# Kernel tuning notes

Hardware: AMD Instinct MI355X
Metric: run time of the kernel (lower is better)

## Reference

```python
import jax, jax.numpy as jnp
import numpy as np

EPS = 1e-5  # config.layer_norm_epsilon

def setup_inputs() -> dict:
    key = jax.random.key(0)
    ks = jax.random.split(key, 3)
    B, S, NX, A, H, O = 16, 2048, 1024, 20, 50, 3
    x = jax.random.normal(ks[0], (B, S, NX), dtype=jnp.float32)
    ln_g = jnp.ones((A, NX), jnp.float32)
    ln_b = jnp.zeros((A, NX), jnp.float32)
    W1 = jax.random.normal(ks[1], (A, NX, H), dtype=jnp.float32) * (1.0 / np.sqrt(NX))
    b1 = jnp.zeros((A, H), jnp.float32)
    W2 = jax.random.normal(ks[2], (A, H, O), dtype=jnp.float32) * (1.0 / np.sqrt(H))
    b2 = jnp.zeros((A, O), jnp.float32)
    return {"x": x, "ln_g": ln_g, "ln_b": ln_b, "W1": W1, "b1": b1, "W2": W2, "b2": b2}

def reference(x, ln_g, ln_b, W1, b1, W2, b2):
    B, S, NX = x.shape
    A = ln_g.shape[0]
    # shared normalization (per-token mean/var), per-adapter affine folded into W1
    mu = jnp.mean(x, axis=-1, keepdims=True)
    var = jnp.mean(jnp.square(x - mu), axis=-1, keepdims=True)  # biased, like torch LN
    xn = (x - mu) * jax.lax.rsqrt(var + EPS)                    # [B,S,NX]
    W1g = ln_g[:, :, None] * W1                                 # [A,NX,H], absorbs LN gamma
    off = jnp.einsum('an,anh->ah', ln_b, W1) + b1               # [A,H],   absorbs LN beta
    h = jax.nn.relu(jnp.einsum('bsn,anh->bash', xn, W1g) + off[None, :, None, :])  # [B,A,S,H]
    o = jnp.einsum('bash,aho->baso', h, W2) + b2[None, :, None, :]                 # [B,A,S,3]
    out = o.reshape(B, A, S * o.shape[-1])                      # [B,A,S*3] (row-major == torch view)
    # squash over the adapter/capsule axis (dim=-1 of [B,S*3,A] == axis 1 here)
    sq = jnp.sum(jnp.square(out), axis=1, keepdims=True)
    scale = sq / (1.0 + sq)
    return scale * out * jax.lax.rsqrt(sq)
```

## Files before the change

### kernel.cpp

```cpp
#include <hip/hip_runtime.h>
#include <hip/hip_bf16.h>
#include <stdint.h>


typedef _Float16 h8 __attribute__((ext_vector_type(8)));
typedef float f4 __attribute__((ext_vector_type(4)));
typedef __attribute__((address_space(1))) void gvoid;
typedef __attribute__((address_space(3))) void lvoid;

__device__ __forceinline__ void cp16(const void* g, void* l) {
  __builtin_amdgcn_global_load_lds((gvoid*)g, (lvoid*)l, 16, 0, 0);
}

__global__ __launch_bounds__(256) void ln_kernel(const float* __restrict__ x,
                                                 _Float16* __restrict__ xn) {
  const int t = threadIdx.x, w = t >> 6, l = t & 63;
  const int tok = blockIdx.x * 4 + w;
  const float4* xr = (const float4*)(x + (size_t)tok * 1024);
  float4 v0 = xr[l * 2], v1 = xr[l * 2 + 1];
  float4 v2 = xr[128 + l * 2], v3 = xr[128 + l * 2 + 1];
  float s1 = (v0.x + v0.y + v0.z + v0.w) + (v1.x + v1.y + v1.z + v1.w) +
             (v2.x + v2.y + v2.z + v2.w) + (v3.x + v3.y + v3.z + v3.w);
  float s2 = v0.x * v0.x + v0.y * v0.y + v0.z * v0.z + v0.w * v0.w;
  s2 += v1.x * v1.x + v1.y * v1.y + v1.z * v1.z + v1.w * v1.w;
  s2 += v2.x * v2.x + v2.y * v2.y + v2.z * v2.z + v2.w * v2.w;
  s2 += v3.x * v3.x + v3.y * v3.y + v3.z * v3.z + v3.w * v3.w;
#pragma unroll
  for (int m = 32; m > 0; m >>= 1) {
    s1 += __shfl_xor(s1, m);
    s2 += __shfl_xor(s2, m);
  }
  const float mu = s1 * 0.0009765625f;
  const float var = s2 * 0.0009765625f - mu * mu;
  const float inv = rsqrtf(var + 1e-5f);
  union { _Float16 h[8]; uint4 u; } p;
  _Float16* xw = xn + (size_t)tok * 1024 + l * 8;
  p.h[0] = (_Float16)((v0.x - mu) * inv); p.h[1] = (_Float16)((v0.y - mu) * inv);
  p.h[2] = (_Float16)((v0.z - mu) * inv); p.h[3] = (_Float16)((v0.w - mu) * inv);
  p.h[4] = (_Float16)((v1.x - mu) * inv); p.h[5] = (_Float16)((v1.y - mu) * inv);
  p.h[6] = (_Float16)((v1.z - mu) * inv); p.h[7] = (_Float16)((v1.w - mu) * inv);
  *(uint4*)xw = p.u;
  p.h[0] = (_Float16)((v2.x - mu) * inv); p.h[1] = (_Float16)((v2.y - mu) * inv);
  p.h[2] = (_Float16)((v2.z - mu) * inv); p.h[3] = (_Float16)((v2.w - mu) * inv);
  p.h[4] = (_Float16)((v3.x - mu) * inv); p.h[5] = (_Float16)((v3.y - mu) * inv);
  p.h[6] = (_Float16)((v3.z - mu) * inv); p.h[7] = (_Float16)((v3.w - mu) * inv);
  *(uint4*)(xw + 512) = p.u;
}

__global__ __launch_bounds__(256) void prep_w(const float* __restrict__ ln_g,
                                              const float* __restrict__ ln_b,
                                              const float* __restrict__ W1,
                                              _Float16* __restrict__ wB,
                                              float* __restrict__ offacc) {
  const int a = blockIdx.x, k0 = blockIdx.y * 64, t = threadIdx.x;
  __shared__ float tw[3200];
  __shared__ float gg[64], bb[64];
  const float* src = W1 + (size_t)(a * 1024 + k0) * 50;
  for (int i = t; i < 3200; i += 256) tw[i] = src[i];
  if (t < 64) gg[t] = ln_g[a * 1024 + k0 + t];
  else if (t < 128) bb[t - 64] = ln_b[a * 1024 + k0 + (t - 64)];
  __syncthreads();
  const int h = t & 63, q = t >> 6;
  float po = 0.f;
#pragma unroll
  for (int half = 0; half < 2; ++half) {
    union { _Float16 hh[8]; uint4 u; } pk;
#pragma unroll
    for (int j = 0; j < 8; ++j) {
      const int k = q * 16 + half * 8 + j;
      float wv = (h < 50) ? tw[k * 50 + h] : 0.f;
      pk.hh[j] = (_Float16)(gg[k] * wv);
      po += bb[k] * wv;
    }
    *(uint4*)(wB + (size_t)(a * 64 + h) * 1024 + k0 + q * 16 + half * 8) =
        pk.u;
  }
  if (h < 50 && po != 0.f) atomicAdd(&offacc[a * 64 + h], po);
}

__global__ __launch_bounds__(256, 4) void gemm_kernel(
    const _Float16* __restrict__ xn, const _Float16* __restrict__ wB,
    const float* __restrict__ offacc, const float* __restrict__ b1,
    const float* __restrict__ W2, const float* __restrict__ b2,
    float* __restrict__ out) {
  __shared__ __align__(16) char smem[35280];
  const int nb = blockIdx.x, mb = blockIdx.y;
  const int t = threadIdx.x, w = t >> 6, l = t & 63;

  float* w2s = (float*)(smem + 34048);
  for (int i = t; i < 300; i += 256) w2s[i] = W2[nb * 300 + i];
  if (t < 6) w2s[300 + t] = b2[nb * 6 + t];

  const int lr = l >> 3;
  const int ksl = (l & 7) ^ lr;
  const _Float16* gA = xn + (size_t)(mb * 128 + lr) * 1024 + ksl * 8;
  const _Float16* gB = wB + (size_t)(nb * 128 + lr) * 1024 + ksl * 8;

  const int rowA = ((w >> 1) * 64) + (l & 15);
  const int rowB = ((w & 1) * 64) + (l & 15);
  const int kq = l >> 4;
  const int xa = rowA & 7, xb = rowB & 7;
  const char* pA = smem + rowA * 128;
  const char* pB = smem + 16384 + rowB * 128;

  f4 acc[4][4];
  {
    f4 z = {0.f, 0.f, 0.f, 0.f};
#pragma unroll
    for (int mt = 0; mt < 4; ++mt)
#pragma unroll
      for (int nt = 0; nt < 4; ++nt) acc[mt][nt] = z;
  }

  for (int kt = 0; kt < 16; ++kt) {
#pragma unroll
    for (int i = 0; i < 4; ++i) {
      const int chunk = w * 4 + i;
      cp16(gA + (size_t)chunk * 8192 + kt * 64, smem + chunk * 1024);
      cp16(gB + (size_t)chunk * 8192 + kt * 64, smem + 16384 + chunk * 1024);
    }
    __syncthreads();
#pragma unroll
    for (int ks = 0; ks < 2; ++ks) {
      h8 af[4], bf[4];
      const int sl = ks * 4 + kq;
#pragma unroll
      for (int mt = 0; mt < 4; ++mt)
        af[mt] = *(const h8*)(pA + mt * 2048 + ((sl ^ xa) << 4));
#pragma unroll
      for (int nt = 0; nt < 4; ++nt)
        bf[nt] = *(const h8*)(pB + nt * 2048 + ((sl ^ xb) << 4));
#pragma unroll
      for (int mt = 0; mt < 4; ++mt)
#pragma unroll
        for (int nt = 0; nt < 4; ++nt)
          acc[mt][nt] = __builtin_amdgcn_mfma_f32_16x16x32_f16(
              af[mt], bf[nt], acc[mt][nt], 0, 0, 0);
    }
    __syncthreads();
  }

  float offt[4];
#pragma unroll
  for (int nt = 0; nt < 4; ++nt) {
    const int nc = rowB + nt * 16;
    const int hh = nc & 63;
    float bv = (hh < 50) ? b1[(nb * 2 + (nc >> 6)) * 50 + hh] : 0.f;
    offt[nt] = offacc[nb * 128 + nc] + bv;
  }

  float* hm = (float*)smem;
  const int mrl = (l >> 4) * 4;
  const int ncol = (w & 1) * 64 + (l & 15);
#pragma unroll
  for (int p = 0; p < 2; ++p) {
    if (p) __syncthreads();
    if ((w >> 1) == p) {
#pragma unroll
      for (int mt = 0; mt < 4; ++mt)
#pragma unroll
        for (int nt = 0; nt < 4; ++nt)
#pragma unroll
          for (int r = 0; r < 4; ++r)
            hm[(mrl + mt * 16 + r) * 133 + (ncol + nt * 16)] =
                fmaxf(acc[mt][nt][r] + offt[nt], 0.f);
    }
    __syncthreads();
    if (t < 128) {
      const int ml = t >> 1, pr = t & 1;
      const float* hrow = hm + ml * 133 + pr * 64;
      const float* wrow = w2s + pr * 150;
      float o0 = w2s[300 + pr * 3 + 0];
      float o1 = w2s[300 + pr * 3 + 1];
      float o2 = w2s[300 + pr * 3 + 2];
#pragma unroll 10
      for (int h = 0; h < 50; ++h) {
        const float hv = hrow[h];
        o0 += hv * wrow[h * 3 + 0];
        o1 += hv * wrow[h * 3 + 1];
        o2 += hv * wrow[h * 3 + 2];
      }
      const int tok = mb * 128 + p * 64 + ml;
      const int b = tok >> 11, s = tok & 2047;
      const int ag = nb * 2 + pr;
      float* op = out + ((size_t)(b * 20 + ag) * 2048 + (size_t)s) * 3;
      op[0] = o0; op[1] = o1; op[2] = o2;
    }
  }
}

__global__ __launch_bounds__(256) void squash_kernel(float* __restrict__ out) {
  const int idx = blockIdx.x * 256 + threadIdx.x;
  const int b = idx / 6144;
  const int rem = idx - b * 6144;
  float v[20];
  float sq = 0.f;
#pragma unroll
  for (int a = 0; a < 20; ++a) {
    v[a] = out[((size_t)(b * 20 + a)) * 6144 + rem];
    sq += v[a] * v[a];
  }
  const float f = sqrtf(sq) / (1.f + sq);
#pragma unroll
  for (int a = 0; a < 20; ++a)
    out[((size_t)(b * 20 + a)) * 6144 + rem] = v[a] * f;
}

extern "C" void kernel_launch(void* const* d_in, const int* in_sizes, int n_in,
                              void* d_out, int out_size, void* d_ws,
                              size_t ws_size, hipStream_t stream) {
  const float* x    = (const float*)d_in[0];
  const float* ln_g = (const float*)d_in[1];
  const float* ln_b = (const float*)d_in[2];
  const float* W1   = (const float*)d_in[3];
  const float* b1   = (const float*)d_in[4];
  const float* W2   = (const float*)d_in[5];
  const float* b2   = (const float*)d_in[6];
  float* out = (float*)d_out;

  char* ws = (char*)d_ws;
  float* offacc = (float*)ws;
  _Float16* wB  = (_Float16*)(ws + 8192);
  _Float16* xnw = (_Float16*)(ws + 8192 + 2621440);

  hipMemsetAsync(offacc, 0, 1280 * sizeof(float), stream);
  prep_w<<<dim3(20, 16), 256, 0, stream>>>(ln_g, ln_b, W1, wB, offacc);
  ln_kernel<<<8192, 256, 0, stream>>>(x, xnw);
  gemm_kernel<<<dim3(10, 256), 256, 0, stream>>>(xnw, wB, offacc, b1, W2, b2, out);
  squash_kernel<<<384, 256, 0, stream>>>(out);
}
```

Measured before the change: 317.6 us.

## Pack adapter columns densely and fuse LayerNorm normalization into GEMM A-tile loads

```diff
diff --git a/kernel.cpp b/kernel.cpp
--- a/kernel.cpp
+++ b/kernel.cpp
@@ -12,39 +12,29 @@
   __builtin_amdgcn_global_load_lds((gvoid*)g, (lvoid*)l, 16, 0, 0);
 }
 
-__global__ __launch_bounds__(256) void ln_kernel(const float* __restrict__ x,
-                                                 _Float16* __restrict__ xn) {
+__global__ __launch_bounds__(256) void stats_kernel(const float* __restrict__ x,
+                                                    float2* __restrict__ st) {
   const int t = threadIdx.x, w = t >> 6, l = t & 63;
   const int tok = blockIdx.x * 4 + w;
   const float4* xr = (const float4*)(x + (size_t)tok * 1024);
-  float4 v0 = xr[l * 2], v1 = xr[l * 2 + 1];
-  float4 v2 = xr[128 + l * 2], v3 = xr[128 + l * 2 + 1];
-  float s1 = (v0.x + v0.y + v0.z + v0.w) + (v1.x + v1.y + v1.z + v1.w) +
-             (v2.x + v2.y + v2.z + v2.w) + (v3.x + v3.y + v3.z + v3.w);
-  float s2 = v0.x * v0.x + v0.y * v0.y + v0.z * v0.z + v0.w * v0.w;
-  s2 += v1.x * v1.x + v1.y * v1.y + v1.z * v1.z + v1.w * v1.w;
-  s2 += v2.x * v2.x + v2.y * v2.y + v2.z * v2.z + v2.w * v2.w;
-  s2 += v3.x * v3.x + v3.y * v3.y + v3.z * v3.z + v3.w * v3.w;
+  float s1 = 0.f, s2 = 0.f;
+#pragma unroll
+  for (int i = 0; i < 4; ++i) {
+    float4 v = xr[l + i * 64];
+    s1 += v.x + v.y + v.z + v.w;
+    s2 += v.x * v.x + v.y * v.y + v.z * v.z + v.w * v.w;
+  }
 #pragma unroll
   for (int m = 32; m > 0; m >>= 1) {
     s1 += __shfl_xor(s1, m);
     s2 += __shfl_xor(s2, m);
   }
-  const float mu = s1 * 0.0009765625f;
-  const float var = s2 * 0.0009765625f - mu * mu;
-  const float inv = rsqrtf(var + 1e-5f);
-  union { _Float16 h[8]; uint4 u; } p;
-  _Float16* xw = xn + (size_t)tok * 1024 + l * 8;
-  p.h[0] = (_Float16)((v0.x - mu) * inv); p.h[1] = (_Float16)((v0.y - mu) * inv);
-  p.h[2] = (_Float16)((v0.z - mu) * inv); p.h[3] = (_Float16)((v0.w - mu) * inv);
-  p.h[4] = (_Float16)((v1.x - mu) * inv); p.h[5] = (_Float16)((v1.y - mu) * inv);
-  p.h[6] = (_Float16)((v1.z - mu) * inv); p.h[7] = (_Float16)((v1.w - mu) * inv);
-  *(uint4*)xw = p.u;
-  p.h[0] = (_Float16)((v2.x - mu) * inv); p.h[1] = (_Float16)((v2.y - mu) * inv);
-  p.h[2] = (_Float16)((v2.z - mu) * inv); p.h[3] = (_Float16)((v2.w - mu) * inv);
-  p.h[4] = (_Float16)((v3.x - mu) * inv); p.h[5] = (_Float16)((v3.y - mu) * inv);
-  p.h[6] = (_Float16)((v3.z - mu) * inv); p.h[7] = (_Float16)((v3.w - mu) * inv);
-  *(uint4*)(xw + 512) = p.u;
+  if (l == 0) {
+    const float mu = s1 * 0.0009765625f;
+    const float var = s2 * 0.0009765625f - mu * mu;
+    const float inv = rsqrtf(var + 1e-5f);
+    st[tok] = make_float2(inv, -mu * inv);
+  }
 }
 
 __global__ __launch_bounds__(256) void prep_w(const float* __restrict__ ln_g,
@@ -61,39 +51,53 @@
   else if (t < 128) bb[t - 64] = ln_b[a * 1024 + k0 + (t - 64)];
   __syncthreads();
   const int h = t & 63, q = t >> 6;
-  float po = 0.f;
-#pragma unroll
-  for (int half = 0; half < 2; ++half) {
-    union { _Float16 hh[8]; uint4 u; } pk;
-#pragma unroll
-    for (int j = 0; j < 8; ++j) {
-      const int k = q * 16 + half * 8 + j;
-      float wv = (h < 50) ? tw[k * 50 + h] : 0.f;
-      pk.hh[j] = (_Float16)(gg[k] * wv);
-      po += bb[k] * wv;
-    }
-    *(uint4*)(wB + (size_t)(a * 64 + h) * 1024 + k0 + q * 16 + half * 8) =
-        pk.u;
-  }
-  if (h < 50 && po != 0.f) atomicAdd(&offacc[a * 64 + h], po);
+  if (h < 50) {
+    float po = 0.f;
+#pragma unroll
+    for (int half = 0; half < 2; ++half) {
+      union { _Float16 hh[8]; uint4 u; } pk;
+#pragma unroll
+      for (int j = 0; j < 8; ++j) {
+        const int k = q * 16 + half * 8 + j;
+        const float wv = tw[k * 50 + h];
+        pk.hh[j] = (_Float16)(gg[k] * wv);
+        po += bb[k] * wv;
+      }
+      *(uint4*)(wB + (size_t)(a * 50 + h) * 1024 + k0 + q * 16 + half * 8) =
+          pk.u;
+    }
+    if (po != 0.f) atomicAdd(&offacc[a * 50 + h], po);
+  }
+  if (a == 0 && t < 192) {
+    const uint4 z = {0, 0, 0, 0};
+    *(uint4*)(wB + (size_t)(1000 + (t >> 3)) * 1024 + k0 + (t & 7) * 8) = z;
+  }
 }
 
 __global__ __launch_bounds__(256, 4) void gemm_kernel(
-    const _Float16* __restrict__ xn, const _Float16* __restrict__ wB,
-    const float* __restrict__ offacc, const float* __restrict__ b1,
-    const float* __restrict__ W2, const float* __restrict__ b2,
+    const float* __restrict__ x, const float2* __restrict__ st,
+    const _Float16* __restrict__ wB, const float* __restrict__ offacc,
+    const float* __restrict__ b1, const float* __restrict__ W2,
     float* __restrict__ out) {
-  __shared__ __align__(16) char smem[35280];
+  __shared__ __align__(16) char smem[36448];
   const int nb = blockIdx.x, mb = blockIdx.y;
   const int t = threadIdx.x, w = t >> 6, l = t & 63;
 
+  const int a0 = (nb * 128) / 50;
   float* w2s = (float*)(smem + 34048);
-  for (int i = t; i < 300; i += 256) w2s[i] = W2[nb * 300 + i];
-  if (t < 6) w2s[300 + t] = b2[nb * 6 + t];
+  for (int i = t; i < 600; i += 256) {
+    const int j = i / 150, a = a0 + j;
+    w2s[i] = (a < 20) ? W2[a * 150 + (i - j * 150)] : 0.f;
+  }
+
+  const int arow = t >> 1, ahf = t & 1;
+  const float2 sb = st[mb * 128 + arow];
+  const float* gx = x + (size_t)(mb * 128 + arow) * 1024 + ahf * 32;
+  char* swA = smem + arow * 128;
+  const int rx = arow & 7;
 
   const int lr = l >> 3;
   const int ksl = (l & 7) ^ lr;
-  const _Float16* gA = xn + (size_t)(mb * 128 + lr) * 1024 + ksl * 8;
   const _Float16* gB = wB + (size_t)(nb * 128 + lr) * 1024 + ksl * 8;
 
   const int rowA = ((w >> 1) * 64) + (l & 15);
@@ -114,10 +118,24 @@
 
   for (int kt = 0; kt < 16; ++kt) {
 #pragma unroll
+    for (int i = 0; i < 4; ++i)
+      cp16(gB + (size_t)(w * 4 + i) * 8192 + kt * 64,
+           smem + 16384 + (w * 4 + i) * 1024);
+    const float4* px = (const float4*)(gx + kt * 64);
+#pragma unroll
     for (int i = 0; i < 4; ++i) {
-      const int chunk = w * 4 + i;
-      cp16(gA + (size_t)chunk * 8192 + kt * 64, smem + chunk * 1024);
-      cp16(gB + (size_t)chunk * 8192 + kt * 64, smem + 16384 + chunk * 1024);
+      const float4 u0 = px[2 * i], u1 = px[2 * i + 1];
+      union { _Float16 hh[8]; uint4 u; } pk;
+      pk.hh[0] = (_Float16)fmaf(u0.x, sb.x, sb.y);
+      pk.hh[1] = (_Float16)fmaf(u0.y, sb.x, sb.y);
+      pk.hh[2] = (_Float16)fmaf(u0.z, sb.x, sb.y);
+      pk.hh[3] = (_Float16)fmaf(u0.w, sb.x, sb.y);
+      pk.hh[4] = (_Float16)fmaf(u1.x, sb.x, sb.y);
+      pk.hh[5] = (_Float16)fmaf(u1.y, sb.x, sb.y);
+      pk.hh[6] = (_Float16)fmaf(u1.z, sb.x, sb.y);
+      pk.hh[7] = (_Float16)fmaf(u1.w, sb.x, sb.y);
+      const int sl = ahf * 4 + i;
+      *(uint4*)(swA + ((sl ^ rx) << 4)) = pk.u;
     }
     __syncthreads();
 #pragma unroll
@@ -143,11 +161,21 @@
   float offt[4];
 #pragma unroll
   for (int nt = 0; nt < 4; ++nt) {
-    const int nc = rowB + nt * 16;
-    const int hh = nc & 63;
-    float bv = (hh < 50) ? b1[(nb * 2 + (nc >> 6)) * 50 + hh] : 0.f;
-    offt[nt] = offacc[nb * 128 + nc] + bv;
-  }
+    const int n = nb * 128 + rowB + nt * 16;
+    offt[nt] = offacc[n] + ((n < 1000) ? b1[n] : 0.f);
+  }
+
+  const int ml = t >> 2, j = t & 3;
+  const int a = a0 + j;
+  const int c0 = nb * 128;
+  int cs = a * 50, ce = cs + 50;
+  if (cs < c0) cs = c0;
+  if (ce > c0 + 128) ce = c0 + 128;
+  const bool act = (a < 20) && (cs < ce);
+  const int lo = cs - c0;
+  const int len = act ? (ce - cs) : 0;
+  const int h0 = cs - a * 50;
+  const float* wrow = w2s + j * 150 + h0 * 3;
 
   float* hm = (float*)smem;
   const int mrl = (l >> 4) * 4;
@@ -166,38 +194,36 @@
                 fmaxf(acc[mt][nt][r] + offt[nt], 0.f);
     }
     __syncthreads();
-    if (t < 128) {
-      const int ml = t >> 1, pr = t & 1;
-      const float* hrow = hm + ml * 133 + pr * 64;
-      const float* wrow = w2s + pr * 150;
-      float o0 = w2s[300 + pr * 3 + 0];
-      float o1 = w2s[300 + pr * 3 + 1];
-      float o2 = w2s[300 + pr * 3 + 2];
-#pragma unroll 10
-      for (int h = 0; h < 50; ++h) {
-        const float hv = hrow[h];
-        o0 += hv * wrow[h * 3 + 0];
-        o1 += hv * wrow[h * 3 + 1];
-        o2 += hv * wrow[h * 3 + 2];
+    if (act) {
+      const float* hr = hm + ml * 133 + lo;
+      float o0 = 0.f, o1 = 0.f, o2 = 0.f;
+      for (int i = 0; i < len; ++i) {
+        const float hv = hr[i];
+        o0 += hv * wrow[i * 3 + 0];
+        o1 += hv * wrow[i * 3 + 1];
+        o2 += hv * wrow[i * 3 + 2];
       }
       const int tok = mb * 128 + p * 64 + ml;
       const int b = tok >> 11, s = tok & 2047;
-      const int ag = nb * 2 + pr;
-      float* op = out + ((size_t)(b * 20 + ag) * 2048 + (size_t)s) * 3;
-      op[0] = o0; op[1] = o1; op[2] = o2;
-    }
-  }
-}
-
-__global__ __launch_bounds__(256) void squash_kernel(float* __restrict__ out) {
+      float* op = out + ((size_t)(b * 20 + a) * 2048 + (size_t)s) * 3;
+      atomicAdd(op + 0, o0);
+      atomicAdd(op + 1, o1);
+      atomicAdd(op + 2, o2);
+    }
+  }
+}
+
+__global__ __launch_bounds__(256) void squash_kernel(float* __restrict__ out,
+                                                     const float* __restrict__ b2) {
   const int idx = blockIdx.x * 256 + threadIdx.x;
   const int b = idx / 6144;
   const int rem = idx - b * 6144;
+  const int oi = rem % 3;
   float v[20];
   float sq = 0.f;
 #pragma unroll
   for (int a = 0; a < 20; ++a) {
-    v[a] = out[((size_t)(b * 20 + a)) * 6144 + rem];
+    v[a] = out[((size_t)(b * 20 + a)) * 6144 + rem] + b2[a * 3 + oi];
     sq += v[a] * v[a];
   }
   const float f = sqrtf(sq) / (1.f + sq);
@@ -220,12 +246,14 @@
 
   char* ws = (char*)d_ws;
   float* offacc = (float*)ws;
-  _Float16* wB  = (_Float16*)(ws + 8192);
-  _Float16* xnw = (_Float16*)(ws + 8192 + 2621440);
-
-  hipMemsetAsync(offacc, 0, 1280 * sizeof(float), stream);
-  prep_w<<<dim3(20, 16), 256, 0, stream>>>(ln_g, ln_b, W1, wB, offacc);
-  ln_kernel<<<8192, 256, 0, stream>>>(x, xnw);
-  gemm_kernel<<<dim3(10, 256), 256, 0, stream>>>(xnw, wB, offacc, b1, W2, b2, out);
-  squash_kernel<<<384, 256, 0, stream>>>(out);
-}
+  float2* stw   = (float2*)(ws + 4096);
+  _Float16* wBw = (_Float16*)(ws + 4096 + 262144);
+
+  hipMemsetAsync(offacc, 0, 1024 * sizeof(float), stream);
+  hipMemsetAsync(out, 0, (size_t)out_size * sizeof(float), stream);
+  stats_kernel<<<8192, 256, 0, stream>>>(x, stw);
+  prep_w<<<dim3(20, 16), 256, 0, stream>>>(ln_g, ln_b, W1, wBw, offacc);
+  gemm_kernel<<<dim3(8, 256), 256, 0, stream>>>(x, stw, wBw, offacc, b1, W2,
+                                                out);
+  squash_kernel<<<384, 256, 0, stream>>>(out, b2);
+}
```

Result: slower. 424.3 us (+33.6%).
